# Performance work log

Hardware: AMD Instinct MI355X
Metric: run time of the kernel (lower is better)

## Reference

```python
import jax, jax.numpy as jnp
import numpy as np
from jax import lax

EPROJS, DUNITS, ATT_DIM = 512, 1024, 320
ACONV_CHANS, ACONV_FILTS = 10, 100
B, T = 64, 2048
SCALING = 2.0


def setup_inputs() -> dict:
    key = jax.random.key(0)
    ks = jax.random.split(key, 10)
    enc_hs_pad = jax.random.normal(ks[0], (B, T, EPROJS), dtype=jnp.float32)
    # lengths in [T//2, T] so no row is fully masked
    enc_hs_len = jax.random.randint(ks[1], (B,), T // 2, T + 1).astype(jnp.int32)
    dec_z = jax.random.normal(ks[2], (B, DUNITS), dtype=jnp.float32)
    att_prev = jax.random.uniform(ks[3], (B, T), dtype=jnp.float32)
    # normalize att_prev like a prob. distribution over valid frames
    att_prev = att_prev / jnp.sum(att_prev, axis=1, keepdims=True)
    s = 0.02
    W_enc = jax.random.normal(ks[4], (ATT_DIM, EPROJS), dtype=jnp.float32) * s
    b_enc = jnp.zeros((ATT_DIM,), dtype=jnp.float32)
    W_dec = jax.random.normal(ks[5], (ATT_DIM, DUNITS), dtype=jnp.float32) * s
    W_att = jax.random.normal(ks[6], (ATT_DIM, ACONV_CHANS), dtype=jnp.float32) * s
    # Conv2d(1, aconv_chans, (1, 2*filts+1)) acts as 1D conv over time
    conv_w = jax.random.normal(ks[7], (ACONV_CHANS, 1, 2 * ACONV_FILTS + 1), dtype=jnp.float32) * s
    W_g = jax.random.normal(ks[8], (1, ATT_DIM), dtype=jnp.float32) * s
    b_g = jnp.zeros((1,), dtype=jnp.float32)
    return {
        "enc_hs_pad": enc_hs_pad, "enc_hs_len": enc_hs_len, "dec_z": dec_z,
        "att_prev": att_prev, "W_enc": W_enc, "b_enc": b_enc, "W_dec": W_dec,
        "W_att": W_att, "conv_w": conv_w, "W_g": W_g, "b_g": b_g,
    }


def reference(enc_hs_pad, enc_hs_len, dec_z, att_prev,
              W_enc, b_enc, W_dec, W_att, conv_w, W_g, b_g):
    # pre_compute_enc_h = mlp_enc(enc_h): [B, T, att_dim]
    pre_enc = jnp.einsum('bte,ae->bta', enc_hs_pad, W_enc) + b_enc
    # location conv: att_prev [B, T] -> [B, C, T] (SAME padding)
    att_conv = lax.conv_general_dilated(
        att_prev[:, None, :], conv_w, window_strides=(1,),
        padding=[(ACONV_FILTS, ACONV_FILTS)],
        dimension_numbers=('NCH', 'OIH', 'NCH'))
    # mlp_att over channels: [B, T, att_dim]
    att_feat = jnp.einsum('bct,ac->bta', att_conv, W_att)
    # mlp_dec(dec_z): [B, 1, att_dim]
    dec_feat = (dec_z @ W_dec.T)[:, None, :]
    # energies: gvec(tanh(sum)) -> [B, T]
    e = jnp.einsum('bta,a->bt', jnp.tanh(att_feat + pre_enc + dec_feat), W_g[0]) + b_g[0]
    # mask padded frames
    t_idx = jnp.arange(e.shape[1])
    pad_mask = t_idx[None, :] >= enc_hs_len[:, None]
    e = jnp.where(pad_mask, -jnp.inf, e)
    w = jax.nn.softmax(SCALING * e, axis=1)
    # context: weighted sum over encoder states -> [B, D_enc]
    c = jnp.einsum('bte,bt->be', enc_hs_pad, w)
    return (c, w)
```

## Files before the change

kernel.cpp:

```cpp
#include <hip/hip_runtime.h>
#include <hip/hip_bf16.h>

#define B_SZ 64
#define T_SZ 2048
#define EPROJS 512
#define DUNITS 1024
#define ATT_DIM 320
#define NCH 10
#define KFILT 201
#define PAD 100

typedef __attribute__((ext_vector_type(8))) __bf16 bf16x8;
typedef __attribute__((ext_vector_type(4))) float f32x4;
typedef __attribute__((ext_vector_type(8))) unsigned short u16x8;

__device__ __forceinline__ unsigned short f2b(float f) {
    __bf16 h = (__bf16)f;
    return __builtin_bit_cast(unsigned short, h);
}

__device__ __forceinline__ void gload_lds16(const void* g, void* l) {
    __builtin_amdgcn_global_load_lds(
        (const __attribute__((address_space(1))) void*)g,
        (__attribute__((address_space(3))) void*)l, 16, 0, 0);
}

__global__ void front_k(const float* __restrict__ W_enc, unsigned short* __restrict__ wbf,
                        const float* __restrict__ dec_z, const float* __restrict__ W_dec,
                        const float* __restrict__ b_enc, float* __restrict__ df,
                        const float* __restrict__ ap, const float* __restrict__ cw,
                        float* __restrict__ conv_out)
{
    __shared__ float s_ap[T_SZ];
    __shared__ float s_cw[KFILT];
    int blk = blockIdx.x, tid = threadIdx.x;

    if (blk < 160) {
        int i = (blk * 256 + tid) * 4;
        float4 v = *(const float4*)(W_enc + i);
        ushort4 o;
        o.x = f2b(v.x); o.y = f2b(v.y); o.z = f2b(v.z); o.w = f2b(v.w);
        *(ushort4*)(wbf + i) = o;
    } else if (blk < 240) {
        int idx = (blk - 160) * 256 + tid;
        int b = idx / ATT_DIM, a = idx - b * ATT_DIM;
        const float4* z = (const float4*)(dec_z + b * DUNITS);
        const float4* w = (const float4*)(W_dec + (size_t)a * DUNITS);
        float s = b_enc[a];
        #pragma unroll 4
        for (int d = 0; d < DUNITS / 4; ++d) {
            float4 zv = z[d], wv = w[d];
            s += zv.x * wv.x + zv.y * wv.y + zv.z * wv.z + zv.w * wv.w;
        }
        df[b * ATT_DIM + a] = s;
    } else {
        int cb = blk - 240;
        int b = cb / NCH, c = cb - b * NCH;
        for (int i = tid; i < T_SZ; i += 256) s_ap[i] = ap[b * T_SZ + i];
        for (int i = tid; i < KFILT; i += 256) s_cw[i] = cw[c * KFILT + i];
        __syncthreads();
        for (int j = 0; j < T_SZ / 256; ++j) {
            int t = tid + j * 256;
            int klo = max(0, PAD - t);
            int khi = min(KFILT, T_SZ + PAD - t);
            float s = 0.f;
            for (int k = klo; k < khi; ++k) s += s_ap[t - PAD + k] * s_cw[k];
            conv_out[((size_t)(b * NCH + c)) * T_SZ + t] = s;
        }
    }
}

__global__ __launch_bounds__(512, 4) void energy_k(
    const float* __restrict__ enc, const unsigned short* __restrict__ wbf,
    const float* __restrict__ df, const float* __restrict__ att_conv,
    const float* __restrict__ W_att, const float* __restrict__ W_g,
    const int* __restrict__ len, float* __restrict__ e_out)
{
    __shared__ unsigned short sW[2][1280 * 8];
    __shared__ float sDf[ATT_DIM], sWg[ATT_DIM], sWatt[ATT_DIM * NCH], sConv[NCH * 128];

    int tid = threadIdx.x;
    int lane = tid & 63, wave = tid >> 6;
    int b = blockIdx.x >> 4;
    int t0 = (blockIdx.x & 15) << 7;

    if (t0 >= len[b]) return;

    int m15 = lane & 15, kg = lane >> 4;
    int row = t0 + wave * 16 + m15;
    const float* aP = enc + ((size_t)b * T_SZ + row) * EPROJS;

    int q0 = tid >> 6;        int g0 = (q0 * 205) >> 10; int wr0 = tid - g0 * 320;
    int i1 = tid + 512;  int q1 = i1 >> 6; int g1 = (q1 * 205) >> 10; int wr1 = i1 - g1 * 320;
    int i2 = tid + 1024; int q2 = i2 >> 6; int g2 = (q2 * 205) >> 10; int wr2 = i2 - g2 * 320;
    bool do2 = tid < 256;
    const unsigned short* wp0 = wbf + (size_t)wr0 * EPROJS + g0 * 8;
    const unsigned short* wp1 = wbf + (size_t)wr1 * EPROJS + g1 * 8;
    const unsigned short* wp2 = wbf + (size_t)wr2 * EPROJS + g2 * 8;

    gload_lds16(wp0, &sW[0][tid * 8]);
    gload_lds16(wp1, &sW[0][i1 * 8]);
    if (do2) gload_lds16(wp2, &sW[0][i2 * 8]);
    float4 a0 = *(const float4*)(aP + kg * 8);
    float4 a1 = *(const float4*)(aP + kg * 8 + 4);

    for (int i = tid; i < ATT_DIM; i += 512) { sDf[i] = df[b * ATT_DIM + i]; sWg[i] = W_g[i]; }
    for (int i = tid; i < ATT_DIM * NCH; i += 512) sWatt[i] = W_att[i];
    for (int i = tid; i < NCH * 128; i += 512)
        sConv[i] = att_conv[((size_t)(b * NCH + (i >> 7))) * T_SZ + t0 + (i & 127)];

    f32x4 acc[20];
    #pragma unroll
    for (int n = 0; n < 20; ++n) acc[n] = (f32x4){0.f, 0.f, 0.f, 0.f};

    __syncthreads();

    for (int t = 0; t < 16; ++t) {
        int cur = t & 1;
        int kn = ((t + 1) & 15) * 32;
        if (t < 15) {
            gload_lds16(wp0 + kn, &sW[cur ^ 1][tid * 8]);
            gload_lds16(wp1 + kn, &sW[cur ^ 1][i1 * 8]);
            if (do2) gload_lds16(wp2 + kn, &sW[cur ^ 1][i2 * 8]);
        }
        float4 n0 = *(const float4*)(aP + kn + kg * 8);
        float4 n1 = *(const float4*)(aP + kn + kg * 8 + 4);

        bf16x8 af;
        af[0] = (__bf16)a0.x; af[1] = (__bf16)a0.y; af[2] = (__bf16)a0.z; af[3] = (__bf16)a0.w;
        af[4] = (__bf16)a1.x; af[5] = (__bf16)a1.y; af[6] = (__bf16)a1.z; af[7] = (__bf16)a1.w;
        const unsigned short* sw = sW[cur];
        #pragma unroll
        for (int nt = 0; nt < 20; ++nt) {
            int wr = nt * 16 + m15;
            bf16x8 wf = *(const bf16x8*)(sw + (kg * 320 + wr) * 8);
            acc[nt] = __builtin_amdgcn_mfma_f32_16x16x32_bf16(af, wf, acc[nt], 0, 0, 0);
        }
        a0 = n0; a1 = n1;

        asm volatile("s_waitcnt vmcnt(2)" ::: "memory");
        __builtin_amdgcn_s_barrier();
    }

    int tl_base = wave * 16 + kg * 4;
    #pragma unroll
    for (int r = 0; r < 4; ++r) {
        int tl = tl_base + r;
        float s = 0.f;
        #pragma unroll
        for (int nt = 0; nt < 20; ++nt) {
            int col = nt * 16 + m15;
            float v = acc[nt][r] + sDf[col];
            float afeat = 0.f;
            #pragma unroll
            for (int c = 0; c < NCH; ++c) afeat += sWatt[col * NCH + c] * sConv[c * 128 + tl];
            v += afeat;
            v = fminf(fmaxf(v, -15.f), 15.f);
            float e2 = __expf(2.f * v);
            s += sWg[col] * ((e2 - 1.f) / (e2 + 1.f));
        }
        s += __shfl_xor(s, 1); s += __shfl_xor(s, 2);
        s += __shfl_xor(s, 4); s += __shfl_xor(s, 8);
        if (m15 == 0) e_out[b * T_SZ + t0 + tl] = s;
    }
}

__global__ void softmax_ctx_k(const float* __restrict__ e, const int* __restrict__ len,
                              const float* __restrict__ enc,
                              float* __restrict__ w_out, float* __restrict__ part) {
    int b = blockIdx.x, tc = blockIdx.y, tid = threadIdx.x;
    int lane = tid & 63, wave = tid >> 6;
    int L = len[b];
    int tb = tc * 128;
    int half = tid >> 7;
    int c4 = tid & 127;
    float* po = part + ((size_t)(b * 32 + tc * 2 + half)) * EPROJS + c4 * 4;

    if (tb >= L) {
        if (tid < 128) w_out[b * T_SZ + tb + tid] = 0.f;
        *(f32x4*)po = (f32x4){0.f, 0.f, 0.f, 0.f};
        return;
    }

    float ev[8];
    float m = -1e30f;
    #pragma unroll
    for (int i = 0; i < 8; ++i) {
        int t = tid + i * 256;
        float x = e[b * T_SZ + t];
        if (t >= L) x = -1e30f;
        ev[i] = x;
        m = fmaxf(m, x);
    }
    #pragma unroll
    for (int o = 32; o > 0; o >>= 1) m = fmaxf(m, __shfl_xor(m, o));
    __shared__ float sred[4];
    if (lane == 0) sred[wave] = m;
    __syncthreads();
    m = fmaxf(fmaxf(sred[0], sred[1]), fmaxf(sred[2], sred[3]));

    float sum = 0.f;
    #pragma unroll
    for (int i = 0; i < 8; ++i) sum += __expf(2.f * (ev[i] - m));
    #pragma unroll
    for (int o = 32; o > 0; o >>= 1) sum += __shfl_xor(sum, o);
    __shared__ float sred2[4];
    if (lane == 0) sred2[wave] = sum;
    __syncthreads();
    sum = sred2[0] + sred2[1] + sred2[2] + sred2[3];
    float inv = 1.f / sum;

    if (tid < 128) {
        int t = tb + tid;
        float wv = 0.f;
        if (t < L) wv = __expf(2.f * (e[b * T_SZ + t] - m)) * inv;
        w_out[b * T_SZ + t] = wv;
    }

    f32x4 s = (f32x4){0.f, 0.f, 0.f, 0.f};
    #pragma unroll 4
    for (int i = half; i < 128; i += 2) {
        int t = tb + i;
        float ee = e[b * T_SZ + t];
        float wv = (t < L) ? __expf(2.f * (ee - m)) * inv : 0.f;
        f32x4 v = *(const f32x4*)(enc + ((size_t)b * T_SZ + t) * EPROJS + c4 * 4);
        s += wv * v;
    }
    *(f32x4*)po = s;
}

__global__ void ctx_reduce_k(const float* __restrict__ part, float* __restrict__ c_out) {
    int b = blockIdx.x;
    int c4 = threadIdx.x;
    f32x4 s = (f32x4){0.f, 0.f, 0.f, 0.f};
    #pragma unroll
    for (int tc = 0; tc < 32; ++tc)
        s += *(const f32x4*)(part + ((size_t)(b * 32 + tc)) * EPROJS + c4 * 4);
    *(f32x4*)(c_out + b * EPROJS + c4 * 4) = s;
}

extern "C" void kernel_launch(void* const* d_in, const int* in_sizes, int n_in,
                              void* d_out, int out_size, void* d_ws, size_t ws_size,
                              hipStream_t stream) {
    const float* enc      = (const float*)d_in[0];
    const int*   len      = (const int*)d_in[1];
    const float* dec_z    = (const float*)d_in[2];
    const float* att_prev = (const float*)d_in[3];
    const float* W_enc    = (const float*)d_in[4];
    const float* b_enc    = (const float*)d_in[5];
    const float* W_dec    = (const float*)d_in[6];
    const float* W_att    = (const float*)d_in[7];
    const float* conv_w   = (const float*)d_in[8];
    const float* W_g      = (const float*)d_in[9];

    char* ws = (char*)d_ws;
    size_t off = 0;
    unsigned short* wbf = (unsigned short*)(ws + off); off += (size_t)ATT_DIM * EPROJS * 2;
    float* e_buf  = (float*)(ws + off); off += (size_t)B_SZ * T_SZ * 4;
    float* dfb    = (float*)(ws + off); off += (size_t)B_SZ * ATT_DIM * 4;
    float* att_cv = (float*)(ws + off); off += (size_t)B_SZ * NCH * T_SZ * 4;
    float* part   = (float*)(ws + off); off += (size_t)B_SZ * 32 * EPROJS * 4;

    float* c_out = (float*)d_out;
    float* w_out = (float*)d_out + B_SZ * EPROJS;

    front_k<<<dim3(880), dim3(256), 0, stream>>>(W_enc, wbf, dec_z, W_dec, b_enc, dfb,
                                                 att_prev, conv_w, att_cv);
    energy_k<<<dim3(B_SZ * 16), dim3(512), 0, stream>>>(enc, wbf, dfb, att_cv, W_att, W_g, len, e_buf);
    softmax_ctx_k<<<dim3(B_SZ, 16), dim3(256), 0, stream>>>(e_buf, len, enc, w_out, part);
    ctx_reduce_k<<<dim3(B_SZ), dim3(128), 0, stream>>>(part, c_out);
}
```

Measured before the change: 252.4 us.

## Stream bf16 W_enc fragments from global into registers instead of LDS double-buffer

The energy kernel no longer stages W_enc tiles in LDS with global_load_lds and per-step barriers. Each lane instead loads its B-operand fragments straight from global (L2-cached) memory into a 10-deep register ring, prefetching ahead of the MFMAs. Blocks shrink to 256 threads covering 64 timesteps, and the grid doubles to match. This removes the barriers and the LDS traffic, but every wave now issues its own weight loads, so cache bandwidth and latency exposure grow and register pressure rises.

```diff
diff --git a/kernel.cpp b/kernel.cpp
--- a/kernel.cpp
+++ b/kernel.cpp
@@ -12,17 +12,10 @@
 
 typedef __attribute__((ext_vector_type(8))) __bf16 bf16x8;
 typedef __attribute__((ext_vector_type(4))) float f32x4;
-typedef __attribute__((ext_vector_type(8))) unsigned short u16x8;
 
 __device__ __forceinline__ unsigned short f2b(float f) {
     __bf16 h = (__bf16)f;
     return __builtin_bit_cast(unsigned short, h);
-}
-
-__device__ __forceinline__ void gload_lds16(const void* g, void* l) {
-    __builtin_amdgcn_global_load_lds(
-        (const __attribute__((address_space(1))) void*)g,
-        (__attribute__((address_space(3))) void*)l, 16, 0, 0);
 }
 
 __global__ void front_k(const float* __restrict__ W_enc, unsigned short* __restrict__ wbf,
@@ -70,44 +63,37 @@
     }
 }
 
-__global__ __launch_bounds__(512, 4) void energy_k(
+__global__ __launch_bounds__(256, 3) void energy_k(
     const float* __restrict__ enc, const unsigned short* __restrict__ wbf,
     const float* __restrict__ df, const float* __restrict__ att_conv,
     const float* __restrict__ W_att, const float* __restrict__ W_g,
     const int* __restrict__ len, float* __restrict__ e_out)
 {
-    __shared__ unsigned short sW[2][1280 * 8];
-    __shared__ float sDf[ATT_DIM], sWg[ATT_DIM], sWatt[ATT_DIM * NCH], sConv[NCH * 128];
+    __shared__ float sDf[ATT_DIM], sWg[ATT_DIM], sWatt[ATT_DIM * NCH], sConv[NCH * 64];
 
     int tid = threadIdx.x;
     int lane = tid & 63, wave = tid >> 6;
-    int b = blockIdx.x >> 4;
-    int t0 = (blockIdx.x & 15) << 7;
+    int b = blockIdx.x >> 5;
+    int t0 = (blockIdx.x & 31) << 6;
 
     if (t0 >= len[b]) return;
 
     int m15 = lane & 15, kg = lane >> 4;
     int row = t0 + wave * 16 + m15;
     const float* aP = enc + ((size_t)b * T_SZ + row) * EPROJS;
-
-    int q0 = tid >> 6;        int g0 = (q0 * 205) >> 10; int wr0 = tid - g0 * 320;
-    int i1 = tid + 512;  int q1 = i1 >> 6; int g1 = (q1 * 205) >> 10; int wr1 = i1 - g1 * 320;
-    int i2 = tid + 1024; int q2 = i2 >> 6; int g2 = (q2 * 205) >> 10; int wr2 = i2 - g2 * 320;
-    bool do2 = tid < 256;
-    const unsigned short* wp0 = wbf + (size_t)wr0 * EPROJS + g0 * 8;
-    const unsigned short* wp1 = wbf + (size_t)wr1 * EPROJS + g1 * 8;
-    const unsigned short* wp2 = wbf + (size_t)wr2 * EPROJS + g2 * 8;
-
-    gload_lds16(wp0, &sW[0][tid * 8]);
-    gload_lds16(wp1, &sW[0][i1 * 8]);
-    if (do2) gload_lds16(wp2, &sW[0][i2 * 8]);
+    const unsigned short* wq = wbf + (size_t)m15 * EPROJS + kg * 8;
+
     float4 a0 = *(const float4*)(aP + kg * 8);
     float4 a1 = *(const float4*)(aP + kg * 8 + 4);
-
-    for (int i = tid; i < ATT_DIM; i += 512) { sDf[i] = df[b * ATT_DIM + i]; sWg[i] = W_g[i]; }
-    for (int i = tid; i < ATT_DIM * NCH; i += 512) sWatt[i] = W_att[i];
-    for (int i = tid; i < NCH * 128; i += 512)
-        sConv[i] = att_conv[((size_t)(b * NCH + (i >> 7))) * T_SZ + t0 + (i & 127)];
+    bf16x8 wf[10];
+    #pragma unroll
+    for (int p = 0; p < 10; ++p)
+        wf[p] = *(const bf16x8*)(wq + p * (16 * EPROJS));
+
+    for (int i = tid; i < ATT_DIM; i += 256) { sDf[i] = df[b * ATT_DIM + i]; sWg[i] = W_g[i]; }
+    for (int i = tid; i < ATT_DIM * NCH; i += 256) sWatt[i] = W_att[i];
+    for (int i = tid; i < NCH * 64; i += 256)
+        sConv[i] = att_conv[((size_t)(b * NCH + (i >> 6))) * T_SZ + t0 + (i & 63)];
 
     f32x4 acc[20];
     #pragma unroll
@@ -116,30 +102,25 @@
     __syncthreads();
 
     for (int t = 0; t < 16; ++t) {
-        int cur = t & 1;
+        int k0 = t * 32;
         int kn = ((t + 1) & 15) * 32;
-        if (t < 15) {
-            gload_lds16(wp0 + kn, &sW[cur ^ 1][tid * 8]);
-            gload_lds16(wp1 + kn, &sW[cur ^ 1][i1 * 8]);
-            if (do2) gload_lds16(wp2 + kn, &sW[cur ^ 1][i2 * 8]);
-        }
         float4 n0 = *(const float4*)(aP + kn + kg * 8);
         float4 n1 = *(const float4*)(aP + kn + kg * 8 + 4);
 
         bf16x8 af;
         af[0] = (__bf16)a0.x; af[1] = (__bf16)a0.y; af[2] = (__bf16)a0.z; af[3] = (__bf16)a0.w;
         af[4] = (__bf16)a1.x; af[5] = (__bf16)a1.y; af[6] = (__bf16)a1.z; af[7] = (__bf16)a1.w;
-        const unsigned short* sw = sW[cur];
+
+        const unsigned short* pc = wq + k0;
+        const unsigned short* pn = wq + kn;
         #pragma unroll
         for (int nt = 0; nt < 20; ++nt) {
-            int wr = nt * 16 + m15;
-            bf16x8 wf = *(const bf16x8*)(sw + (kg * 320 + wr) * 8);
-            acc[nt] = __builtin_amdgcn_mfma_f32_16x16x32_bf16(af, wf, acc[nt], 0, 0, 0);
+            bf16x8 wcur = wf[nt % 10];
+            if (nt < 10) wf[nt % 10] = *(const bf16x8*)(pc + (nt + 10) * (16 * EPROJS));
+            else         wf[nt % 10] = *(const bf16x8*)(pn + (nt - 10) * (16 * EPROJS));
+            acc[nt] = __builtin_amdgcn_mfma_f32_16x16x32_bf16(af, wcur, acc[nt], 0, 0, 0);
         }
         a0 = n0; a1 = n1;
-
-        asm volatile("s_waitcnt vmcnt(2)" ::: "memory");
-        __builtin_amdgcn_s_barrier();
     }
 
     int tl_base = wave * 16 + kg * 4;
@@ -153,7 +134,7 @@
             float v = acc[nt][r] + sDf[col];
             float afeat = 0.f;
             #pragma unroll
-            for (int c = 0; c < NCH; ++c) afeat += sWatt[col * NCH + c] * sConv[c * 128 + tl];
+            for (int c = 0; c < NCH; ++c) afeat += sWatt[col * NCH + c] * sConv[c * 64 + tl];
             v += afeat;
             v = fminf(fmaxf(v, -15.f), 15.f);
             float e2 = __expf(2.f * v);
@@ -266,7 +247,7 @@
 
     front_k<<<dim3(880), dim3(256), 0, stream>>>(W_enc, wbf, dec_z, W_dec, b_enc, dfb,
                                                  att_prev, conv_w, att_cv);
-    energy_k<<<dim3(B_SZ * 16), dim3(512), 0, stream>>>(enc, wbf, dfb, att_cv, W_att, W_g, len, e_buf);
+    energy_k<<<dim3(B_SZ * 32), dim3(256), 0, stream>>>(enc, wbf, dfb, att_cv, W_att, W_g, len, e_buf);
     softmax_ctx_k<<<dim3(B_SZ, 16), dim3(256), 0, stream>>>(e_buf, len, enc, w_out, part);
     ctx_reduce_k<<<dim3(B_SZ), dim3(128), 0, stream>>>(part, c_out);
 }
```

New measurement: 464.9 us. +84.2%, slower.
